# Kernel tuning notes

Measured on AMD Instinct MI355X. Metric: run time of the kernel, lower is better.

## Reference

```python
import jax, jax.numpy as jnp
import numpy as np

N_HOURLY = 24
D_MODEL = 512
D_POOL = D_MODEL // 4  # 128


def setup_inputs() -> dict:
    key = jax.random.key(0)
    ks = jax.random.split(key, 9)
    B, E, D = 64, 2048, D_MODEL
    day_embed = jax.random.normal(ks[0], (B, D), dtype=jnp.float32)
    episode_ctx = jax.random.normal(ks[1], (B, E, D), dtype=jnp.float32)
    n_episodes = jax.random.randint(ks[2], (B,), 0, E)
    d_in = D + N_HOURLY * D_POOL  # 3584
    W_pool = jax.random.normal(ks[3], (D, D_POOL), dtype=jnp.float32) * (1.0 / np.sqrt(D))
    b_pool = jnp.zeros((D_POOL,), dtype=jnp.float32)
    W1 = jax.random.normal(ks[4], (d_in, D), dtype=jnp.float32) * (1.0 / np.sqrt(d_in))
    b1 = jnp.zeros((D,), dtype=jnp.float32)
    W2 = jax.random.normal(ks[5], (D, 2), dtype=jnp.float32) * (1.0 / np.sqrt(D))
    b2 = jnp.zeros((2,), dtype=jnp.float32)
    return {"day_embed": day_embed, "episode_ctx": episode_ctx, "n_episodes": n_episodes,
            "W_pool": W_pool, "b_pool": b_pool, "W1": W1, "b1": b1, "W2": W2, "b2": b2}


def reference(day_embed, episode_ctx, n_episodes, W_pool, b_pool, W1, b1, W2, b2):
    B, E, D = episode_ctx.shape
    # project all (padded) episodes: [B, E, D/4]
    feats = jnp.einsum('bed,dk->bek', episode_ctx, W_pool) + b_pool
    # bin_size = max(n_ep // 24, 1); episode j (j < n_ep) belongs to bin j // bin_size,
    # dropped if bin >= 24. This exactly reproduces the torch slicing loop.
    bs = jnp.maximum(n_episodes // N_HOURLY, 1)  # [B]
    j = jnp.arange(E)
    bin_id = j[None, :] // bs[:, None]                       # [B, E]
    valid = (j[None, :] < n_episodes[:, None]) & (bin_id < N_HOURLY)
    hmask = (bin_id[:, None, :] == jnp.arange(N_HOURLY)[None, :, None]) & valid[:, None, :]
    mf = hmask.astype(feats.dtype)                           # [B, H, E]
    sums = jnp.einsum('bhe,bek->bhk', mf, feats)             # [B, H, D/4]
    counts = mf.sum(-1)                                      # [B, H]
    hourly = jnp.where(counts[..., None] > 0,
                       sums / jnp.maximum(counts, 1.0)[..., None],
                       jnp.zeros_like(sums))
    x = jnp.concatenate([day_embed, hourly.reshape(B, -1)], axis=-1)  # [B, 3584]
    h = jax.nn.gelu(x @ W1 + b1, approximate=False)  # torch nn.GELU default = exact erf
    return h @ W2 + b2  # [B, 2]; dropout is identity in eval mode
```

## Files before the change

### kernel.cpp

```cpp
#include <hip/hip_runtime.h>
#include <math.h>

#define NH    24
#define DM    512
#define DP    128
#define EMAX  2048
#define DIN   3584
#define B     64
#define SLABS 32
#define SROWS 112


__global__ void binpool_kernel(const float* __restrict__ day_embed,
                               const float* __restrict__ episode_ctx,
                               const int* __restrict__ n_episodes,
                               const float* __restrict__ W_pool,
                               const float* __restrict__ b_pool,
                               float* __restrict__ x_T) {
    const int h = blockIdx.x;
    const int b = blockIdx.y;
    const int t = threadIdx.x;

    if (h == NH) {
        for (int i = t; i < DM; i += 256)
            x_T[(size_t)i * B + b] = day_embed[b * DM + i];
        return;
    }

    const int n  = n_episodes[b];
    int bs = n / NH; if (bs < 1) bs = 1;
    const int lo = h * bs;
    int hi = lo + bs; if (hi > n) hi = n;
    int count = hi - lo; if (count < 0) count = 0;

    __shared__ float4 sh4[256];
    __shared__ float  sh_mean[DM];
    __shared__ float4 redp4[8][32];

    const int p  = t & 127;
    const int eo = t >> 7;

    float4 a = make_float4(0.f, 0.f, 0.f, 0.f);
    const float4* base = (const float4*)episode_ctx
                       + (size_t)b * EMAX * (DM / 4) + p;
    #pragma unroll 4
    for (int e = lo + eo; e < hi; e += 2) {
        float4 v = base[(size_t)e * (DM / 4)];
        a.x += v.x; a.y += v.y; a.z += v.z; a.w += v.w;
    }
    sh4[t] = a;
    __syncthreads();

    if (t < 128) {
        const float inv = (count > 0) ? (1.0f / (float)count) : 0.0f;
        float4 u = sh4[t], v = sh4[t + 128];
        sh_mean[4 * t]     = (u.x + v.x) * inv;
        sh_mean[4 * t + 1] = (u.y + v.y) * inv;
        sh_mean[4 * t + 2] = (u.z + v.z) * inv;
        sh_mean[4 * t + 3] = (u.w + v.w) * inv;
    }
    __syncthreads();

    {
        const int g    = t >> 6;
        const int lane = t & 63;
        const int dh   = lane >> 5;
        const int kq   = lane & 31;
        float4 acc = make_float4(0.f, 0.f, 0.f, 0.f);
        const float4* wp4 = (const float4*)W_pool + kq;
        const int d0 = g * 128 + dh;
        #pragma unroll 8
        for (int di = 0; di < 64; ++di) {
            const int d = d0 + 2 * di;
            float  m = sh_mean[d];
            float4 w = wp4[(size_t)d * (DP / 4)];
            acc.x += m * w.x; acc.y += m * w.y;
            acc.z += m * w.z; acc.w += m * w.w;
        }
        redp4[2 * g + dh][kq] = acc;
    }
    __syncthreads();

    if (t < DP) {
        const float* rp = (const float*)redp4;
        float v = 0.f;
        #pragma unroll
        for (int r = 0; r < 8; ++r) v += rp[r * DP + t];
        const int row = DM + h * DP + t;
        x_T[(size_t)row * B + b] = (count > 0) ? (v + b_pool[t]) : 0.f;
    }
}

__global__ void mlp1_kernel(const float* __restrict__ x_T,
                            const float* __restrict__ W1,
                            float* __restrict__ part) {
    const int c = blockIdx.x;
    const int s = blockIdx.y;
    const int t = threadIdx.x;
    const int w = t >> 6;
    const int lane = t & 63;

    float acc[16];
    #pragma unroll
    for (int j = 0; j < 16; ++j) acc[j] = 0.f;

    const int k0 = SROWS * s + 28 * w;
    const float4* wbase = (const float4*)(W1 + (size_t)k0 * DM + 16 * c);
    const float* xbase = x_T + (size_t)k0 * B + lane;

    #pragma unroll 4
    for (int ki = 0; ki < 28; ++ki) {
        float xv = xbase[ki * B];
        const float4* wrow = wbase + (size_t)ki * (DM / 4);
        #pragma unroll
        for (int q = 0; q < 4; ++q) {
            float4 wv = wrow[q];
            acc[4 * q]     += xv * wv.x;
            acc[4 * q + 1] += xv * wv.y;
            acc[4 * q + 2] += xv * wv.z;
            acc[4 * q + 3] += xv * wv.w;
        }
    }

    __shared__ float red[4][64][17];
    #pragma unroll
    for (int j = 0; j < 16; ++j)
        red[w][lane][j] = acc[j];
    __syncthreads();

    for (int idx = t; idx < 1024; idx += 256) {
        const int row = idx >> 4;
        const int j   = idx & 15;
        float v = red[0][row][j] + red[1][row][j] + red[2][row][j] + red[3][row][j];
        part[(size_t)s * (B * DM) + (size_t)row * DM + 16 * c + j] = v;
    }
}

__global__ void tail_kernel(const float* __restrict__ part,
                            const float* __restrict__ b1,
                            const float* __restrict__ W2,
                            const float* __restrict__ b2,
                            float* __restrict__ out) {
    const int b = blockIdx.x;
    const int t = threadIdx.x;

    __shared__ float sh_h[DM];

    #pragma unroll
    for (int rep = 0; rep < 2; ++rep) {
        const int col = t + rep * 256;
        float v0 = 0.f, v1 = 0.f;
        #pragma unroll
        for (int s = 0; s < SLABS; s += 2) {
            v0 += part[(size_t)s * (B * DM) + (size_t)b * DM + col];
            v1 += part[(size_t)(s + 1) * (B * DM) + (size_t)b * DM + col];
        }
        float v = v0 + v1 + b1[col];
        sh_h[col] = 0.5f * v * (1.0f + erff(v * 0.70710678118654752f));
    }
    __syncthreads();

    if (t < 64) {
        float a0 = 0.f, a1 = 0.f;
        #pragma unroll
        for (int i = t; i < DM; i += 64) {
            float hv = sh_h[i];
            float2 w = ((const float2*)W2)[i];
            a0 += hv * w.x;
            a1 += hv * w.y;
        }
        #pragma unroll
        for (int off = 32; off > 0; off >>= 1) {
            a0 += __shfl_down(a0, off);
            a1 += __shfl_down(a1, off);
        }
        if (t == 0) {
            out[b * 2]     = a0 + b2[0];
            out[b * 2 + 1] = a1 + b2[1];
        }
    }
}

extern "C" void kernel_launch(void* const* d_in, const int* in_sizes, int n_in,
                              void* d_out, int out_size, void* d_ws, size_t ws_size,
                              hipStream_t stream) {
    const float* day_embed   = (const float*)d_in[0];
    const float* episode_ctx = (const float*)d_in[1];
    const int*   n_episodes  = (const int*)d_in[2];
    const float* W_pool      = (const float*)d_in[3];
    const float* b_pool      = (const float*)d_in[4];
    const float* W1          = (const float*)d_in[5];
    const float* b1          = (const float*)d_in[6];
    const float* W2          = (const float*)d_in[7];
    const float* b2          = (const float*)d_in[8];
    float* out = (float*)d_out;

    float* x_T  = (float*)d_ws;
    float* part = x_T + (size_t)DIN * B;

    dim3 gA(NH + 1, B);
    binpool_kernel<<<gA, 256, 0, stream>>>(day_embed, episode_ctx, n_episodes,
                                           W_pool, b_pool, x_T);
    dim3 gB(32, SLABS);
    mlp1_kernel<<<gB, 256, 0, stream>>>(x_T, W1, part);

    tail_kernel<<<64, 256, 0, stream>>>(part, b1, W2, b2, out);
}
```

Before: 381.2 us.

## Fuse tail reduction into MLP kernel via last-block atomic counters

Removes the separate tail kernel. The last slab block for each column chunk, detected with an atomic counter, sums the split-K partials, applies bias and GELU, and computes partial W2 products. A second counter lets the final column block reduce those products into the output. Counters are zeroed inside binpool, and launch bounds are added to both kernels. This saves a kernel launch and its pass over the partials, at the cost of threadfences and atomics plus a serialized tail in the last blocks.

```diff
diff --git a/kernel.cpp b/kernel.cpp
--- a/kernel.cpp
+++ b/kernel.cpp
@@ -11,17 +11,20 @@
 #define SROWS 112
 
 
-__global__ void binpool_kernel(const float* __restrict__ day_embed,
-                               const float* __restrict__ episode_ctx,
-                               const int* __restrict__ n_episodes,
-                               const float* __restrict__ W_pool,
-                               const float* __restrict__ b_pool,
-                               float* __restrict__ x_T) {
+__global__ __launch_bounds__(256, 6)
+void binpool_kernel(const float* __restrict__ day_embed,
+                    const float* __restrict__ episode_ctx,
+                    const int* __restrict__ n_episodes,
+                    const float* __restrict__ W_pool,
+                    const float* __restrict__ b_pool,
+                    float* __restrict__ x_T,
+                    int* __restrict__ cnts) {
     const int h = blockIdx.x;
     const int b = blockIdx.y;
     const int t = threadIdx.x;
 
     if (h == NH) {
+        if (b == 0 && t < 33) cnts[t] = 0;
         for (int i = t; i < DM; i += 256)
             x_T[(size_t)i * B + b] = day_embed[b * DM + i];
         return;
@@ -91,9 +94,16 @@
     }
 }
 
-__global__ void mlp1_kernel(const float* __restrict__ x_T,
-                            const float* __restrict__ W1,
-                            float* __restrict__ part) {
+__global__ __launch_bounds__(256, 4)
+void mlp_kernel(const float* __restrict__ x_T,
+                const float* __restrict__ W1,
+                const float* __restrict__ b1,
+                const float* __restrict__ W2,
+                const float* __restrict__ b2,
+                float* __restrict__ part,
+                float* __restrict__ pc,
+                int* __restrict__ cnts,
+                float* __restrict__ out) {
     const int c = blockIdx.x;
     const int s = blockIdx.y;
     const int t = threadIdx.x;
@@ -123,6 +133,7 @@
     }
 
     __shared__ float red[4][64][17];
+    __shared__ int   s_rank;
     #pragma unroll
     for (int j = 0; j < 16; ++j)
         red[w][lane][j] = acc[j];
@@ -134,50 +145,57 @@
         float v = red[0][row][j] + red[1][row][j] + red[2][row][j] + red[3][row][j];
         part[(size_t)s * (B * DM) + (size_t)row * DM + 16 * c + j] = v;
     }
-}
-
-__global__ void tail_kernel(const float* __restrict__ part,
-                            const float* __restrict__ b1,
-                            const float* __restrict__ W2,
-                            const float* __restrict__ b2,
-                            float* __restrict__ out) {
-    const int b = blockIdx.x;
-    const int t = threadIdx.x;
-
-    __shared__ float sh_h[DM];
-
-    #pragma unroll
-    for (int rep = 0; rep < 2; ++rep) {
-        const int col = t + rep * 256;
-        float v0 = 0.f, v1 = 0.f;
-        #pragma unroll
-        for (int s = 0; s < SLABS; s += 2) {
-            v0 += part[(size_t)s * (B * DM) + (size_t)b * DM + col];
-            v1 += part[(size_t)(s + 1) * (B * DM) + (size_t)b * DM + col];
-        }
-        float v = v0 + v1 + b1[col];
-        sh_h[col] = 0.5f * v * (1.0f + erff(v * 0.70710678118654752f));
-    }
-    __syncthreads();
-
-    if (t < 64) {
+
+    __threadfence();
+    __syncthreads();
+    if (t == 0) s_rank = atomicAdd(&cnts[c], 1);
+    __syncthreads();
+    if (s_rank != SLABS - 1) return;
+
+    __threadfence();
+    {
+        const int fb = t >> 2;
+        const int cq = t & 3;
+        const int col0 = 16 * c + 4 * cq;
+        const float* pp = part + (size_t)fb * DM + col0;
+        float4 a4 = make_float4(0.f, 0.f, 0.f, 0.f);
+        #pragma unroll 8
+        for (int sl = 0; sl < SLABS; ++sl) {
+            float4 v = *(const float4*)(pp + (size_t)sl * (B * DM));
+            a4.x += v.x; a4.y += v.y; a4.z += v.z; a4.w += v.w;
+        }
+        float vv[4] = {a4.x, a4.y, a4.z, a4.w};
         float a0 = 0.f, a1 = 0.f;
         #pragma unroll
-        for (int i = t; i < DM; i += 64) {
-            float hv = sh_h[i];
-            float2 w = ((const float2*)W2)[i];
-            a0 += hv * w.x;
-            a1 += hv * w.y;
-        }
-        #pragma unroll
-        for (int off = 32; off > 0; off >>= 1) {
-            a0 += __shfl_down(a0, off);
-            a1 += __shfl_down(a1, off);
-        }
-        if (t == 0) {
-            out[b * 2]     = a0 + b2[0];
-            out[b * 2 + 1] = a1 + b2[1];
-        }
+        for (int k2 = 0; k2 < 4; ++k2) {
+            float v = vv[k2] + b1[col0 + k2];
+            float g = 0.5f * v * (1.0f + erff(v * 0.70710678118654752f));
+            a0 += g * W2[(col0 + k2) * 2];
+            a1 += g * W2[(col0 + k2) * 2 + 1];
+        }
+        a0 += __shfl_down(a0, 2, 4); a0 += __shfl_down(a0, 1, 4);
+        a1 += __shfl_down(a1, 2, 4); a1 += __shfl_down(a1, 1, 4);
+        if (cq == 0) {
+            pc[((size_t)c * B + fb) * 2]     = a0;
+            pc[((size_t)c * B + fb) * 2 + 1] = a1;
+        }
+    }
+
+    __threadfence();
+    __syncthreads();
+    if (t == 0) s_rank = atomicAdd(&cnts[32], 1);
+    __syncthreads();
+    if (s_rank != 31) return;
+
+    __threadfence();
+    if (t < 128) {
+        const int fb = t >> 1;
+        const int j  = t & 1;
+        float v = b2[j];
+        #pragma unroll 8
+        for (int cc = 0; cc < 32; ++cc)
+            v += pc[((size_t)cc * B + fb) * 2 + j];
+        out[fb * 2 + j] = v;
     }
 }
 
@@ -197,12 +215,12 @@
 
     float* x_T  = (float*)d_ws;
     float* part = x_T + (size_t)DIN * B;
+    float* pc   = part + (size_t)SLABS * B * DM;
+    int*   cnts = (int*)(pc + 32 * B * 2);
 
     dim3 gA(NH + 1, B);
     binpool_kernel<<<gA, 256, 0, stream>>>(day_embed, episode_ctx, n_episodes,
-                                           W_pool, b_pool, x_T);
+                                           W_pool, b_pool, x_T, cnts);
     dim3 gB(32, SLABS);
-    mlp1_kernel<<<gB, 256, 0, stream>>>(x_T, W1, part);
-
-    tail_kernel<<<64, 256, 0, stream>>>(part, b1, W2, b2, out);
+    mlp_kernel<<<gB, 256, 0, stream>>>(x_T, W1, b1, W2, b2, part, pc, cnts, out);
 }
```

Result: slower. 484.2 us (+27.0%).
